# Optimization experiments

Measured on AMD Instinct MI355X. Metric: run time of the kernel, lower is better.

## Reference

```python
import jax, jax.numpy as jnp
import numpy as np

ALPHA = 0.1  # blend factor from init

def grid_sample_bilinear(tex, grid):
    # tex: [B,C,H,W]; grid: [B,Ho,Wo,2] with (x,y) in [-1,1].
    # Matches torch F.grid_sample(mode='bilinear', padding_mode='zeros', align_corners=False).
    B, C, H, W = tex.shape
    Ho, Wo = grid.shape[1], grid.shape[2]
    ix = ((grid[..., 0] + 1.0) * W - 1.0) * 0.5
    iy = ((grid[..., 1] + 1.0) * H - 1.0) * 0.5
    x0 = jnp.floor(ix); y0 = jnp.floor(iy)
    x1 = x0 + 1.0;      y1 = y0 + 1.0
    wx1 = ix - x0; wx0 = 1.0 - wx1
    wy1 = iy - y0; wy0 = 1.0 - wy1
    flat = tex.reshape(B, C, H * W).transpose(0, 2, 1)  # [B, H*W, C]

    def gather(xf, yf):
        valid = ((xf >= 0) & (xf < W) & (yf >= 0) & (yf < H)).astype(tex.dtype)
        xi = jnp.clip(xf.astype(jnp.int32), 0, W - 1)
        yi = jnp.clip(yf.astype(jnp.int32), 0, H - 1)
        idx = (yi * W + xi).reshape(B, Ho * Wo)
        v = jnp.take_along_axis(flat, idx[:, :, None], axis=1)  # [B, N, C]
        return v * valid.reshape(B, Ho * Wo)[:, :, None]

    w00 = (wx0 * wy0).reshape(B, -1)[:, :, None]
    w10 = (wx1 * wy0).reshape(B, -1)[:, :, None]
    w01 = (wx0 * wy1).reshape(B, -1)[:, :, None]
    w11 = (wx1 * wy1).reshape(B, -1)[:, :, None]
    out = (gather(x0, y0) * w00 + gather(x1, y0) * w10 +
           gather(x0, y1) * w01 + gather(x1, y1) * w11)  # [B, N, C]
    return out.reshape(B, Ho, Wo, C).transpose(0, 3, 1, 2)

def bicubic_grid_sample(tex, grid):
    # 5-tap Catmull-Rom approximation of bicubic filtering (matches BiCubicGridSample).
    B, C, H, W = tex.shape
    wsz = jnp.asarray([W, H], dtype=tex.dtype)
    rws = 1.0 / wsz
    uv = (grid + 1.0) * 0.5
    pos = uv * wsz
    cpos = jnp.floor(pos - 0.5) + 0.5
    f = pos - cpos; f2 = f * f; f3 = f2 * f
    w0 = -0.5 * f3 + f2 - 0.5 * f
    w1 = 1.5 * f3 - 2.5 * f2 + 1.0
    w2 = -1.5 * f3 + 2.0 * f2 + 0.5 * f
    w3 = 0.5 * f3 - 0.5 * f2
    w12 = w1 + w2
    tc12 = rws * (cpos + w2 / w12)
    tc0 = rws * (cpos - 1.0)
    tc3 = rws * (cpos + 2.0)

    def samp(u, v):
        uvg = jnp.stack((u, v), axis=-1)
        return grid_sample_bilinear(tex, (uvg - 0.5) * 2.0)  # UVToGrid

    # 5 taps in the plus pattern, with the per-tap scalar weights (alpha channel is a
    # constant 1 in the original, so the denominator is just the sum of the weights).
    k1 = w12[..., 0] * w0[..., 1]
    k2 = w0[..., 0] * w12[..., 1]
    k3 = w3[..., 0] * w12[..., 1]
    k4 = w12[..., 0] * w3[..., 1]
    k5 = w12[..., 0] * w12[..., 1]
    rgb = (samp(tc12[..., 0], tc0[..., 1]) * k1[:, None] +
           samp(tc0[..., 0], tc12[..., 1]) * k2[:, None] +
           samp(tc3[..., 0], tc12[..., 1]) * k3[:, None] +
           samp(tc12[..., 0], tc3[..., 1]) * k4[:, None] +
           samp(tc12[..., 0], tc12[..., 1]) * k5[:, None])
    denom = (k1 + k2 + k3 + k4 + k5)[:, None]
    return jnp.clip(rgb / denom, 0.0, 1.0)

def max_pool3(x):
    # 3x3 max pool, stride 1, padding 1 (SAME) on NCHW.
    return jax.lax.reduce_window(x, -jnp.inf, jax.lax.max,
                                 (1, 1, 3, 3), (1, 1, 1, 1), 'SAME')

def setup_inputs() -> dict:
    key = jax.random.key(0)
    k1, k2, k3 = jax.random.split(key, 3)
    B, C, H, W = 4, 3, 1080, 1920
    x = jax.random.uniform(k1, (B, C, H, W), dtype=jnp.float32)
    mv = jax.random.uniform(k2, (B, H, W, 2), dtype=jnp.float32)  # in [0,1) subset of [-1,1]
    history = jax.random.uniform(k3, (B, C, H, W), dtype=jnp.float32)
    return {"x": x, "mv": mv, "history": history}

def reference(x, mv, history):
    # TAA forward, steady-state (history present), use_bic=True, hist_clamp=True.
    rep = bicubic_grid_sample(history, mv)
    max_nh = max_pool3(x)
    min_nh = -max_pool3(-x)
    rep = jnp.minimum(jnp.maximum(rep, min_nh), max_nh)  # neighborhood clamp
    return ALPHA * x + (1.0 - ALPHA) * rep
```

## Files before the change

### kernel.cpp

```cpp
#include <hip/hip_runtime.h>

namespace {

constexpr int Bn = 4, Cn = 3, Hn = 1080, Wn = 1920;
constexpr int HW = Hn * Wn;
constexpr float kAlpha = 0.1f;
constexpr float kInv2047 = 1.0f / 2047.0f;
constexpr float kInv1023 = 1.0f / 1023.0f;
constexpr int kPad = 16;

typedef float v2f __attribute__((ext_vector_type(2)));
typedef float v4f __attribute__((ext_vector_type(4)));
typedef unsigned int v4u __attribute__((ext_vector_type(4)));
typedef unsigned int v4u_u __attribute__((ext_vector_type(4), aligned(4)));
typedef unsigned int v2u_u __attribute__((ext_vector_type(2), aligned(4)));

__device__ inline unsigned quant_rgb(float r, float g, float b)
{
    const unsigned R  = (unsigned)(fminf(fmaxf(r, 0.0f), 1.0f) * 2047.0f + 0.5f);
    const unsigned G  = (unsigned)(fminf(fmaxf(g, 0.0f), 1.0f) * 2047.0f + 0.5f);
    const unsigned Bq = (unsigned)(fminf(fmaxf(b, 0.0f), 1.0f) * 1023.0f + 0.5f);
    return (R << 21) | (G << 10) | Bq;
}

__global__ __launch_bounds__(256)
void pack_linear(const float* __restrict__ hist, unsigned int* __restrict__ packed)
{
    const int tid = blockIdx.x * 256 + threadIdx.x;
    const int b   = tid / (HW / 4);
    const int r   = tid - b * (HW / 4);

    const float* base = hist + (size_t)b * Cn * HW + (size_t)r * 4;
    const v4f rr = *(const v4f*)(base);
    const v4f gg = *(const v4f*)(base + HW);
    const v4f bb = *(const v4f*)(base + 2 * HW);

    v4u t;
    t.x = quant_rgb(rr.x, gg.x, bb.x);
    t.y = quant_rgb(rr.y, gg.y, bb.y);
    t.z = quant_rgb(rr.z, gg.z, bb.z);
    t.w = quant_rgb(rr.w, gg.w, bb.w);
    *(v4u*)(packed + (size_t)b * HW + (size_t)r * 4) = t;
}

__device__ inline void bicubic_gather_lin(const unsigned int* __restrict__ pp,
                                          float gx, float gy, float rep[3])
{
    const float posx = (gx + 1.0f) * 0.5f * (float)Wn;
    const float posy = (gy + 1.0f) * 0.5f * (float)Hn;
    const float Xf = floorf(posx - 0.5f);
    const float Yf = floorf(posy - 0.5f);
    const float fx = posx - (Xf + 0.5f);
    const float fy = posy - (Yf + 0.5f);

    const float fx2 = fx * fx, fx3 = fx2 * fx;
    const float w0x = -0.5f * fx3 + fx2 - 0.5f * fx;
    const float w1x =  1.5f * fx3 - 2.5f * fx2 + 1.0f;
    const float w2x = -1.5f * fx3 + 2.0f * fx2 + 0.5f * fx;
    const float w3x =  0.5f * fx3 - 0.5f * fx2;
    const float w12x = w1x + w2x;
    const float bxr  = w2x / w12x;

    const float fy2 = fy * fy, fy3 = fy2 * fy;
    const float w0y = -0.5f * fy3 + fy2 - 0.5f * fy;
    const float w1y =  1.5f * fy3 - 2.5f * fy2 + 1.0f;
    const float w2y = -1.5f * fy3 + 2.0f * fy2 + 0.5f * fy;
    const float w3y =  0.5f * fy3 - 0.5f * fy2;
    const float w12y = w1y + w2y;
    const float byr  = w2y / w12y;

    const int X = (int)Xf;
    const int Y = (int)Yf;

    const float vxm1 = ((unsigned)(X - 1) < (unsigned)Wn) ? 1.0f : 0.0f;
    const float vx0  = ((unsigned)(X    ) < (unsigned)Wn) ? 1.0f : 0.0f;
    const float vx1  = ((unsigned)(X + 1) < (unsigned)Wn) ? 1.0f : 0.0f;
    const float vx2  = ((unsigned)(X + 2) < (unsigned)Wn) ? 1.0f : 0.0f;
    const float vym1 = ((unsigned)(Y - 1) < (unsigned)Hn) ? 1.0f : 0.0f;
    const float vy0  = ((unsigned)(Y    ) < (unsigned)Hn) ? 1.0f : 0.0f;
    const float vy1  = ((unsigned)(Y + 1) < (unsigned)Hn) ? 1.0f : 0.0f;
    const float vy2  = ((unsigned)(Y + 2) < (unsigned)Hn) ? 1.0f : 0.0f;

    const float k1 = w12x * w0y;
    const float k2 = w0x * w12y;
    const float k3 = w3x * w12y;
    const float k4 = w12x * w3y;
    const float k5 = w12x * w12y;
    const float inv_denom = 1.0f / (k1 + k2 + k3 + k4 + k5);

    const float wxl = 1.0f - bxr, wxh = bxr;
    const float wyl = 1.0f - byr, wyh = byr;

    const float wA = k1 * wxl * (vym1 * vx0);
    const float wB = k1 * wxh * (vym1 * vx1);
    const float wC = k2 * wyl * (vxm1 * vy0);
    const float wD = k2 * wyh * (vxm1 * vy1);
    const float wE = k3 * wyl * (vx2 * vy0);
    const float wF = k3 * wyh * (vx2 * vy1);
    const float wG = k4 * wxl * (vy2 * vx0);
    const float wH = k4 * wxh * (vy2 * vx1);
    const float wI = k5 * wxl * wyl * (vx0 * vy0);
    const float wJ = k5 * wxh * wyl * (vx1 * vy0);
    const float wK = k5 * wxl * wyh * (vx0 * vy1);
    const float wL = k5 * wxh * wyh * (vx1 * vy1);

    const int W0  = X - 1;
    const int rYm = min(max(Y - 1, 0), Hn - 1) * Wn;
    const int rY0 = min(max(Y,     0), Hn - 1) * Wn;
    const int rY1 = min(max(Y + 1, 0), Hn - 1) * Wn;
    const int rY2 = min(max(Y + 2, 0), Hn - 1) * Wn;

    const v4u_u R0 = *(const v4u_u*)(pp + rY0 + W0);
    const v4u_u R1 = *(const v4u_u*)(pp + rY1 + W0);
    const v2u_u Rm = *(const v2u_u*)(pp + rYm + X);
    const v2u_u R2 = *(const v2u_u*)(pp + rY2 + X);

    float accR = 0.0f, accG = 0.0f, accB = 0.0f;
#define TAA_TAP(w_, t_) {                                                   \
    accR = fmaf(w_, (float)((t_) >> 21),           accR);                   \
    accG = fmaf(w_, (float)(((t_) >> 10) & 2047u), accG);                   \
    accB = fmaf(w_, (float)((t_) & 1023u),         accB); }
    TAA_TAP(wA, Rm.x) TAA_TAP(wB, Rm.y) TAA_TAP(wC, R0.x) TAA_TAP(wD, R1.x)
    TAA_TAP(wE, R0.w) TAA_TAP(wF, R1.w) TAA_TAP(wG, R2.x) TAA_TAP(wH, R2.y)
    TAA_TAP(wI, R0.y) TAA_TAP(wJ, R0.z) TAA_TAP(wK, R1.y) TAA_TAP(wL, R1.z)
#undef TAA_TAP
    rep[0] = accR * (kInv2047 * inv_denom);
    rep[1] = accG * (kInv2047 * inv_denom);
    rep[2] = accB * (kInv1023 * inv_denom);
}

__global__ __launch_bounds__(128)
void taa_main_lin(const float* __restrict__ xin,
                  const v2f* __restrict__ mv,
                  const unsigned int* __restrict__ packed,
                  float* __restrict__ out)
{
    const int bid = blockIdx.x;
    const int b   = bid & 3;
    const int r   = bid >> 2;
    const int u   = r * 128 + threadIdx.x;
    const int py  = u / 960;
    const int P   = (u - py * 960) * 2;
    const int p   = py * Wn + P;

    const v4f gg = __builtin_nontemporal_load((const v4f*)&mv[(size_t)b * HW + p]);

    const unsigned int* __restrict__ pp = packed + (size_t)b * HW;
    float rep0[3], rep1[3];
    bicubic_gather_lin(pp, gg.x, gg.y, rep0);
    bicubic_gather_lin(pp, gg.z, gg.w, rep1);

    const int pym = max(py - 1, 0) * Wn;
    const int py0 = py * Wn;
    const int pyp = min(py + 1, Hn - 1) * Wn;
    const int lane = threadIdx.x & 63;

    float ctr0[3], ctr1[3];
    float mxlo[3], mxhi[3], mnlo[3], mnhi[3];
    #pragma unroll
    for (int c = 0; c < Cn; ++c) {
        const float* __restrict__ xp = xin + (size_t)(b * Cn + c) * HW;
        const v2f a = *(const v2f*)(xp + pym + P);
        const v2f m = *(const v2f*)(xp + py0 + P);
        const v2f z = *(const v2f*)(xp + pyp + P);
        ctr0[c] = m.x; ctr1[c] = m.y;
        mxlo[c] = fmaxf(fmaxf(a.x, m.x), z.x);
        mxhi[c] = fmaxf(fmaxf(a.y, m.y), z.y);
        mnlo[c] = fminf(fminf(a.x, m.x), z.x);
        mnhi[c] = fminf(fminf(a.y, m.y), z.y);
    }

    float lmx[3], lmn[3], rmx[3], rmn[3];
    #pragma unroll
    for (int c = 0; c < Cn; ++c) {
        lmx[c] = __shfl_up(mxhi[c], 1);
        lmn[c] = __shfl_up(mnhi[c], 1);
        rmx[c] = __shfl_down(mxlo[c], 1);
        rmn[c] = __shfl_down(mnlo[c], 1);
    }

    if (lane == 0 || lane == 63) {
        const int ex = (lane == 0) ? max(P - 1, 0) : min(P + 2, Wn - 1);
        #pragma unroll
        for (int c = 0; c < Cn; ++c) {
            const float* __restrict__ xp = xin + (size_t)(b * Cn + c) * HW;
            const float e0 = xp[pym + ex];
            const float e1 = xp[py0 + ex];
            const float e2 = xp[pyp + ex];
            const float emax = fmaxf(fmaxf(e0, e1), e2);
            const float emin = fminf(fminf(e0, e1), e2);
            if (lane == 0) { lmx[c] = emax; lmn[c] = emin; }
            else           { rmx[c] = emax; rmn[c] = emin; }
        }
    }

    #pragma unroll
    for (int c = 0; c < Cn; ++c) {
        const float mx0 = fmaxf(fmaxf(lmx[c], mxlo[c]), mxhi[c]);
        const float mn0 = fminf(fminf(lmn[c], mnlo[c]), mnhi[c]);
        const float mx1 = fmaxf(fmaxf(mxlo[c], mxhi[c]), rmx[c]);
        const float mn1 = fminf(fminf(mnlo[c], mnhi[c]), rmn[c]);

        float rv0 = fminf(fmaxf(rep0[c], 0.0f), 1.0f);
        float rv1 = fminf(fmaxf(rep1[c], 0.0f), 1.0f);
        rv0 = fminf(fmaxf(rv0, mn0), mx0);
        rv1 = fminf(fmaxf(rv1, mn1), mx1);

        v2f o;
        o.x = kAlpha * ctr0[c] + (1.0f - kAlpha) * rv0;
        o.y = kAlpha * ctr1[c] + (1.0f - kAlpha) * rv1;
        __builtin_nontemporal_store(o, (v2f*)&out[(size_t)(b * Cn + c) * HW + p]);
    }
}

__global__ __launch_bounds__(128)
void taa_fallback(const float* __restrict__ xin,
                  const v2f* __restrict__ mv,
                  const float* __restrict__ hist,
                  float* __restrict__ out)
{
    const int bid = blockIdx.x;
    const int b   = bid & 3;
    const int rr  = bid >> 2;
    const int py  = rr / 15;
    const int px  = (rr - py * 15) * 128 + threadIdx.x;
    const int p   = py * Wn + px;

    const v2f g = mv[(size_t)b * HW + p];
    const float posx = (g.x + 1.0f) * 0.5f * (float)Wn;
    const float posy = (g.y + 1.0f) * 0.5f * (float)Hn;
    const float Xf = floorf(posx - 0.5f);
    const float Yf = floorf(posy - 0.5f);
    const float fx = posx - (Xf + 0.5f);
    const float fy = posy - (Yf + 0.5f);
    const float fx2 = fx * fx, fx3 = fx2 * fx;
    const float w0x = -0.5f * fx3 + fx2 - 0.5f * fx;
    const float w1x =  1.5f * fx3 - 2.5f * fx2 + 1.0f;
    const float w2x = -1.5f * fx3 + 2.0f * fx2 + 0.5f * fx;
    const float w3x =  0.5f * fx3 - 0.5f * fx2;
    const float w12x = w1x + w2x, bxr = w2x / w12x;
    const float fy2 = fy * fy, fy3 = fy2 * fy;
    const float w0y = -0.5f * fy3 + fy2 - 0.5f * fy;
    const float w1y =  1.5f * fy3 - 2.5f * fy2 + 1.0f;
    const float w2y = -1.5f * fy3 + 2.0f * fy2 + 0.5f * fy;
    const float w3y =  0.5f * fy3 - 0.5f * fy2;
    const float w12y = w1y + w2y, byr = w2y / w12y;
    const int X = (int)Xf, Y = (int)Yf;
    const float vxm1 = ((unsigned)(X - 1) < (unsigned)Wn) ? 1.0f : 0.0f;
    const float vx0  = ((unsigned)(X    ) < (unsigned)Wn) ? 1.0f : 0.0f;
    const float vx1  = ((unsigned)(X + 1) < (unsigned)Wn) ? 1.0f : 0.0f;
    const float vx2  = ((unsigned)(X + 2) < (unsigned)Wn) ? 1.0f : 0.0f;
    const float vym1 = ((unsigned)(Y - 1) < (unsigned)Hn) ? 1.0f : 0.0f;
    const float vy0  = ((unsigned)(Y    ) < (unsigned)Hn) ? 1.0f : 0.0f;
    const float vy1  = ((unsigned)(Y + 1) < (unsigned)Hn) ? 1.0f : 0.0f;
    const float vy2  = ((unsigned)(Y + 2) < (unsigned)Hn) ? 1.0f : 0.0f;
    const float k1 = w12x * w0y, k2 = w0x * w12y, k3 = w3x * w12y;
    const float k4 = w12x * w3y, k5 = w12x * w12y;
    const float inv_denom = 1.0f / (k1 + k2 + k3 + k4 + k5);
    const float wxl = 1.0f - bxr, wxh = bxr, wyl = 1.0f - byr, wyh = byr;
    const float wA = k1 * wxl * (vym1 * vx0), wB = k1 * wxh * (vym1 * vx1);
    const float wC = k2 * wyl * (vxm1 * vy0), wD = k2 * wyh * (vxm1 * vy1);
    const float wE = k3 * wyl * (vx2 * vy0),  wF = k3 * wyh * (vx2 * vy1);
    const float wG = k4 * wxl * (vy2 * vx0),  wH = k4 * wxh * (vy2 * vx1);
    const float wI = k5 * wxl * wyl * (vx0 * vy0), wJ = k5 * wxh * wyl * (vx1 * vy0);
    const float wK = k5 * wxl * wyh * (vx0 * vy1), wL = k5 * wxh * wyh * (vx1 * vy1);
    const int cxm1 = min(max(X - 1, 0), Wn - 1), cx0 = min(max(X, 0), Wn - 1);
    const int cx1 = min(max(X + 1, 0), Wn - 1),  cx2 = min(max(X + 2, 0), Wn - 1);
    const int rym1 = min(max(Y - 1, 0), Hn - 1) * Wn, ry0 = min(max(Y, 0), Hn - 1) * Wn;
    const int ry1 = min(max(Y + 1, 0), Hn - 1) * Wn,  ry2 = min(max(Y + 2, 0), Hn - 1) * Wn;

    const int pym = max(py - 1, 0) * Wn;
    const int py0 = py * Wn;
    const int pyp = min(py + 1, Hn - 1) * Wn;
    const int pxm = max(px - 1, 0);
    const int pxp = min(px + 1, Wn - 1);

    #pragma unroll
    for (int c = 0; c < Cn; ++c) {
        const size_t plane = (size_t)(b * Cn + c) * HW;
        const float* __restrict__ hp = hist + plane;
        float acc = wA * hp[rym1 + cx0];
        acc = fmaf(wB, hp[rym1 + cx1], acc);
        acc = fmaf(wC, hp[ry0 + cxm1], acc);
        acc = fmaf(wD, hp[ry1 + cxm1], acc);
        acc = fmaf(wE, hp[ry0 + cx2], acc);
        acc = fmaf(wF, hp[ry1 + cx2], acc);
        acc = fmaf(wG, hp[ry2 + cx0], acc);
        acc = fmaf(wH, hp[ry2 + cx1], acc);
        acc = fmaf(wI, hp[ry0 + cx0], acc);
        acc = fmaf(wJ, hp[ry0 + cx1], acc);
        acc = fmaf(wK, hp[ry1 + cx0], acc);
        acc = fmaf(wL, hp[ry1 + cx1], acc);
        float rv = fminf(fmaxf(acc * inv_denom, 0.0f), 1.0f);

        const float* __restrict__ xp = xin + plane;
        const float r0a = xp[pym + pxm], r0b = xp[pym + px], r0c = xp[pym + pxp];
        const float r1a = xp[py0 + pxm], r1b = xp[py0 + px], r1c = xp[py0 + pxp];
        const float r2a = xp[pyp + pxm], r2b = xp[pyp + px], r2c = xp[pyp + pxp];
        const float mx = fmaxf(fmaxf(fmaxf(r0a, r0b), fmaxf(r0c, r1a)),
                               fmaxf(fmaxf(r1b, r1c), fmaxf(fmaxf(r2a, r2b), r2c)));
        const float mn = fminf(fminf(fminf(r0a, r0b), fminf(r0c, r1a)),
                               fminf(fminf(r1b, r1c), fminf(fminf(r2a, r2b), r2c)));
        rv = fminf(fmaxf(rv, mn), mx);
        out[plane + p] = kAlpha * r1b + (1.0f - kAlpha) * rv;
    }
}

}

extern "C" void kernel_launch(void* const* d_in, const int* in_sizes, int n_in,
                              void* d_out, int out_size, void* d_ws, size_t ws_size,
                              hipStream_t stream) {
    const float* x    = (const float*)d_in[0];
    const v2f*   mv   = (const v2f*)d_in[1];
    const float* hist = (const float*)d_in[2];
    float* outp = (float*)d_out;

    const size_t lin_bytes = ((size_t)Bn * HW + 2 * kPad) * 4;

    if (ws_size >= lin_bytes) {
        unsigned int* packed = (unsigned int*)d_ws + kPad;
        pack_linear<<<Bn * HW / 4 / 256, 256, 0, stream>>>(hist, packed);
        taa_main_lin<<<Bn * HW / 256, 128, 0, stream>>>(x, mv, packed, outp);
    } else {
        taa_fallback<<<(Wn / 128) * Hn * Bn, 128, 0, stream>>>(x, mv, hist, outp);
    }
}
```

Before: 419.8 us.

## Pack history into row-pair interleaved layout for fewer gather loads

Replaces the linear packed-history layout with one that interleaves each pair of rows, so vertically adjacent texels sit next to each other in memory. The bicubic gather now issues four 16-byte loads covering the 12 taps and picks texels with parity-based selects, in place of two 16-byte plus two 8-byte unaligned row loads. This aims to cut the number of distinct cache lines and memory transactions per sample. In exchange it adds select logic, more complex addressing and clamping, and a workspace padded by one extra row pair per image.

```diff
diff --git a/kernel.cpp b/kernel.cpp
--- a/kernel.cpp
+++ b/kernel.cpp
@@ -4,6 +4,8 @@
 
 constexpr int Bn = 4, Cn = 3, Hn = 1080, Wn = 1920;
 constexpr int HW = Hn * Wn;
+constexpr int Qn = Hn / 2;
+constexpr int PRSTRIDE = (Qn + 1) * Wn * 2;
 constexpr float kAlpha = 0.1f;
 constexpr float kInv2047 = 1.0f / 2047.0f;
 constexpr float kInv1023 = 1.0f / 1023.0f;
@@ -12,8 +14,7 @@
 typedef float v2f __attribute__((ext_vector_type(2)));
 typedef float v4f __attribute__((ext_vector_type(4)));
 typedef unsigned int v4u __attribute__((ext_vector_type(4)));
-typedef unsigned int v4u_u __attribute__((ext_vector_type(4), aligned(4)));
-typedef unsigned int v2u_u __attribute__((ext_vector_type(2), aligned(4)));
+typedef unsigned int v4u_u __attribute__((ext_vector_type(4), aligned(8)));
 
 __device__ inline unsigned quant_rgb(float r, float g, float b)
 {
@@ -24,27 +25,36 @@
 }
 
 __global__ __launch_bounds__(256)
-void pack_linear(const float* __restrict__ hist, unsigned int* __restrict__ packed)
+void pack_pairs(const float* __restrict__ hist, unsigned int* __restrict__ packed)
 {
     const int tid = blockIdx.x * 256 + threadIdx.x;
-    const int b   = tid / (HW / 4);
-    const int r   = tid - b * (HW / 4);
-
-    const float* base = hist + (size_t)b * Cn * HW + (size_t)r * 4;
-    const v4f rr = *(const v4f*)(base);
-    const v4f gg = *(const v4f*)(base + HW);
-    const v4f bb = *(const v4f*)(base + 2 * HW);
-
-    v4u t;
-    t.x = quant_rgb(rr.x, gg.x, bb.x);
-    t.y = quant_rgb(rr.y, gg.y, bb.y);
-    t.z = quant_rgb(rr.z, gg.z, bb.z);
-    t.w = quant_rgb(rr.w, gg.w, bb.w);
-    *(v4u*)(packed + (size_t)b * HW + (size_t)r * 4) = t;
-}
-
-__device__ inline void bicubic_gather_lin(const unsigned int* __restrict__ pp,
-                                          float gx, float gy, float rep[3])
+    const int g   = tid % (Wn / 4);
+    const int rem = tid / (Wn / 4);
+    const int q   = rem % Qn;
+    const int b   = rem / Qn;
+    const int x0  = g * 4;
+
+    const float* base = hist + (size_t)b * Cn * HW + (size_t)(2 * q) * Wn + x0;
+    const v4f r0 = *(const v4f*)(base);
+    const v4f g0 = *(const v4f*)(base + HW);
+    const v4f b0 = *(const v4f*)(base + 2 * HW);
+    const v4f r1 = *(const v4f*)(base + Wn);
+    const v4f g1 = *(const v4f*)(base + Wn + HW);
+    const v4f b1 = *(const v4f*)(base + Wn + 2 * HW);
+
+    v4u lo, hi;
+    #pragma unroll
+    for (int i = 0; i < 4; ++i) {
+        lo[i] = quant_rgb(r0[i], g0[i], b0[i]);
+        hi[i] = quant_rgb(r1[i], g1[i], b1[i]);
+    }
+    unsigned int* dst = packed + (size_t)b * PRSTRIDE + ((size_t)q * Wn + x0) * 2;
+    *(v4u*)(dst)     = (v4u){lo.x, hi.x, lo.y, hi.y};
+    *(v4u*)(dst + 4) = (v4u){lo.z, hi.z, lo.w, hi.w};
+}
+
+__device__ inline void bicubic_gather_pair(const unsigned int* __restrict__ pp,
+                                           float gx, float gy, float rep[3])
 {
     const float posx = (gx + 1.0f) * 0.5f * (float)Wn;
     const float posy = (gy + 1.0f) * 0.5f * (float)Hn;
@@ -104,25 +114,43 @@
     const float wK = k5 * wxl * wyh * (vx0 * vy1);
     const float wL = k5 * wxh * wyh * (vx1 * vy1);
 
-    const int W0  = X - 1;
-    const int rYm = min(max(Y - 1, 0), Hn - 1) * Wn;
-    const int rY0 = min(max(Y,     0), Hn - 1) * Wn;
-    const int rY1 = min(max(Y + 1, 0), Hn - 1) * Wn;
-    const int rY2 = min(max(Y + 2, 0), Hn - 1) * Wn;
-
-    const v4u_u R0 = *(const v4u_u*)(pp + rY0 + W0);
-    const v4u_u R1 = *(const v4u_u*)(pp + rY1 + W0);
-    const v2u_u Rm = *(const v2u_u*)(pp + rYm + X);
-    const v2u_u R2 = *(const v2u_u*)(pp + rY2 + X);
+    const int q   = Y >> 1;
+    const int par = Y & 1;
+    const int qA  = min(max(q,     0), Qn);
+    const int qB  = min(max(q + 1, 0), Qn);
+    const int qC  = min(max(q - 1, 0), Qn);
+
+    const int eA  = (qA * Wn + (X - 1)) * 2;
+    const int eL2 = par ? (qB * Wn + (X - 1)) * 2 : (qC * Wn + X) * 2;
+    const int eL3 = par ? (qB * Wn + (X + 1)) * 2 : (qB * Wn + X) * 2;
+
+    const v4u_u A0 = *(const v4u_u*)(pp + eA);
+    const v4u_u A1 = *(const v4u_u*)(pp + eA + 4);
+    const v4u_u L2 = *(const v4u_u*)(pp + eL2);
+    const v4u_u L3 = *(const v4u_u*)(pp + eL3);
+
+    const bool od = (par != 0);
+    const unsigned tA = od ? A0.z : L2.y;
+    const unsigned tB = od ? A1.x : L2.w;
+    const unsigned tC = od ? A0.y : A0.x;
+    const unsigned tD = od ? L2.x : A0.y;
+    const unsigned tE = od ? A1.w : A1.z;
+    const unsigned tF = od ? L3.z : A1.w;
+    const unsigned tG = od ? L2.w : L3.x;
+    const unsigned tH = od ? L3.y : L3.z;
+    const unsigned tI = od ? A0.w : A0.z;
+    const unsigned tJ = od ? A1.y : A1.x;
+    const unsigned tK = od ? L2.z : A0.w;
+    const unsigned tL = od ? L3.x : A1.y;
 
     float accR = 0.0f, accG = 0.0f, accB = 0.0f;
 #define TAA_TAP(w_, t_) {                                                   \
     accR = fmaf(w_, (float)((t_) >> 21),           accR);                   \
     accG = fmaf(w_, (float)(((t_) >> 10) & 2047u), accG);                   \
     accB = fmaf(w_, (float)((t_) & 1023u),         accB); }
-    TAA_TAP(wA, Rm.x) TAA_TAP(wB, Rm.y) TAA_TAP(wC, R0.x) TAA_TAP(wD, R1.x)
-    TAA_TAP(wE, R0.w) TAA_TAP(wF, R1.w) TAA_TAP(wG, R2.x) TAA_TAP(wH, R2.y)
-    TAA_TAP(wI, R0.y) TAA_TAP(wJ, R0.z) TAA_TAP(wK, R1.y) TAA_TAP(wL, R1.z)
+    TAA_TAP(wA, tA) TAA_TAP(wB, tB) TAA_TAP(wC, tC) TAA_TAP(wD, tD)
+    TAA_TAP(wE, tE) TAA_TAP(wF, tF) TAA_TAP(wG, tG) TAA_TAP(wH, tH)
+    TAA_TAP(wI, tI) TAA_TAP(wJ, tJ) TAA_TAP(wK, tK) TAA_TAP(wL, tL)
 #undef TAA_TAP
     rep[0] = accR * (kInv2047 * inv_denom);
     rep[1] = accG * (kInv2047 * inv_denom);
@@ -130,10 +158,10 @@
 }
 
 __global__ __launch_bounds__(128)
-void taa_main_lin(const float* __restrict__ xin,
-                  const v2f* __restrict__ mv,
-                  const unsigned int* __restrict__ packed,
-                  float* __restrict__ out)
+void taa_main_pair(const float* __restrict__ xin,
+                   const v2f* __restrict__ mv,
+                   const unsigned int* __restrict__ packed,
+                   float* __restrict__ out)
 {
     const int bid = blockIdx.x;
     const int b   = bid & 3;
@@ -145,10 +173,10 @@
 
     const v4f gg = __builtin_nontemporal_load((const v4f*)&mv[(size_t)b * HW + p]);
 
-    const unsigned int* __restrict__ pp = packed + (size_t)b * HW;
+    const unsigned int* __restrict__ pp = packed + (size_t)b * PRSTRIDE;
     float rep0[3], rep1[3];
-    bicubic_gather_lin(pp, gg.x, gg.y, rep0);
-    bicubic_gather_lin(pp, gg.z, gg.w, rep1);
+    bicubic_gather_pair(pp, gg.x, gg.y, rep0);
+    bicubic_gather_pair(pp, gg.z, gg.w, rep1);
 
     const int pym = max(py - 1, 0) * Wn;
     const int py0 = py * Wn;
@@ -316,12 +344,12 @@
     const float* hist = (const float*)d_in[2];
     float* outp = (float*)d_out;
 
-    const size_t lin_bytes = ((size_t)Bn * HW + 2 * kPad) * 4;
-
-    if (ws_size >= lin_bytes) {
+    const size_t pair_bytes = ((size_t)Bn * PRSTRIDE + 2 * kPad) * 4;
+
+    if (ws_size >= pair_bytes) {
         unsigned int* packed = (unsigned int*)d_ws + kPad;
-        pack_linear<<<Bn * HW / 4 / 256, 256, 0, stream>>>(hist, packed);
-        taa_main_lin<<<Bn * HW / 256, 128, 0, stream>>>(x, mv, packed, outp);
+        pack_pairs<<<Bn * Qn * (Wn / 4) / 256, 256, 0, stream>>>(hist, packed);
+        taa_main_pair<<<Bn * HW / 256, 128, 0, stream>>>(x, mv, packed, outp);
     } else {
         taa_fallback<<<(Wn / 128) * Hn * Bn, 128, 0, stream>>>(x, mv, hist, outp);
     }
```

Measured after the change: 406.8 us. 3.1% less time.
